# Performance work log

Hardware: AMD Instinct MI355X
Metric: run time of the kernel (lower is better)

Reference implementation:

```python
import jax, jax.numpy as jnp
import numpy as np

NUM_HEADS = 8
NEG_INF = -1e30


def _within_bucket_rank(idx):
    # idx: [U] int32 bucket ids; returns occurrence count of each id among earlier positions
    U = idx.shape[0]
    order = jnp.argsort(idx, stable=True)
    sv = idx[order]
    pos = jnp.arange(U, dtype=jnp.int32)
    is_start = jnp.concatenate([jnp.ones((1,), bool), sv[1:] != sv[:-1]])
    start = jax.lax.cummax(jnp.where(is_start, pos, 0))
    rank = pos - start
    return jnp.zeros(U, jnp.int32).at[order].set(rank)


def setup_inputs() -> dict:
    key = jax.random.key(0)
    ks = jax.random.split(key, 10)
    B, U, G, E = 8, 16384, 64, 128
    lin = jnp.linspace(0.0, 1.0, G)
    gx, gy = jnp.meshgrid(lin, lin, indexing='ij')
    xc_on_grid = jnp.broadcast_to(jnp.stack([gx, gy], -1), (B, G, G, 2)).astype(jnp.float32)
    s = 0.02
    return {
        'xc_off_grid': jax.random.uniform(ks[0], (B, U, 2), jnp.float32),
        'xc_on_grid': xc_on_grid,
        'zc_off_grid': jax.random.normal(ks[1], (B, U, E), jnp.float32),
        'zc_on_grid': jax.random.normal(ks[2], (B, G, G, E), jnp.float32),
        'latents': jax.random.normal(ks[3], (G * G, E), jnp.float32),
        'fake_embedding': jax.random.normal(ks[4], (E,), jnp.float32),
        'Wq': jax.random.normal(ks[5], (E, E), jnp.float32) * s,
        'Wk': jax.random.normal(ks[6], (E, E), jnp.float32) * s,
        'Wv': jax.random.normal(ks[7], (E, E), jnp.float32) * s,
        'Wo': jax.random.normal(ks[8], (E, E), jnp.float32) * s,
        'ignore_on_grid': 0,
    }


def _bucketize(xc_off_grid, xc_on_grid):
    # returns nearest flat grid index per off-grid point, shape [B, U] int32
    B = xc_off_grid.shape[0]
    dims = xc_on_grid.shape[1:-1]
    S = int(np.prod(dims))
    grid_shape = jnp.asarray(dims, jnp.float32)
    x_on = xc_on_grid.reshape(B, S, -1)
    xmin = x_on.min(axis=(0, 1))
    xmax = x_on.max(axis=(0, 1))
    spacing = (xmax - xmin) / (grid_shape - 1.0)
    nm = jnp.floor((xc_off_grid - xmin + spacing / 2) / spacing)
    nm = jnp.clip(nm, 0.0, grid_shape - 1.0)
    # strides as in the original: flip(cumprod([1, *dims])[:-1])
    strides = np.flip(np.cumprod(np.concatenate([[1], np.asarray(dims)]))[:-1]).astype(np.float32)
    return (nm * jnp.asarray(strides)).sum(-1).astype(jnp.int32)


def _mhca(latents_q, kv, valid, Wq, Wk, Wv, Wo):
    # latents_q: [N,1,E], kv: [N,P,E], valid: [N,P] bool
    N, P, E = kv.shape
    H, Dh = NUM_HEADS, E // NUM_HEADS
    q = (latents_q @ Wq).reshape(N, 1, H, Dh)
    k = (kv @ Wk).reshape(N, P, H, Dh)
    v = (kv @ Wv).reshape(N, P, H, Dh)
    scores = jnp.einsum('nqhd,nkhd->nhqk', q, k) / jnp.sqrt(jnp.asarray(Dh, q.dtype))
    scores = jnp.where(valid[:, None, None, :], scores, NEG_INF)
    attn = jax.nn.softmax(scores, axis=-1)
    out = jnp.einsum('nhqk,nkhd->nqhd', attn, v).reshape(N, 1, E)
    return out @ Wo


def reference(xc_off_grid, xc_on_grid, zc_off_grid, zc_on_grid, latents, fake_embedding, Wq, Wk, Wv, Wo, ignore_on_grid):
    B, U, E = zc_off_grid.shape
    dims = xc_on_grid.shape[1:-1]
    S = int(np.prod(dims))
    z_on = zc_on_grid.reshape(B, S, E)

    nearest_idx = _bucketize(xc_off_grid, xc_on_grid)          # [B, U]
    cumcount = jax.vmap(_within_bucket_rank)(nearest_idx)       # [B, U]
    flat_seg = (nearest_idx + jnp.arange(B, dtype=jnp.int32)[:, None] * S).reshape(-1)
    counts = jax.ops.segment_sum(jnp.ones(B * U, jnp.int32), flat_seg, num_segments=B * S)
    max_patch = int(jax.device_get(counts.max())) + 1           # +1 slot for on-grid/fake token

    # ragged scatter of off-grid tokens into padded per-bucket buffer
    grid_stacked = jnp.zeros((B * S, max_patch, E), zc_off_grid.dtype)
    grid_stacked = grid_stacked.at[flat_seg, cumcount.reshape(-1)].set(zc_off_grid.reshape(B * U, E))
    if ignore_on_grid:
        last = jnp.broadcast_to(fake_embedding, (B * S, E))
    else:
        last = z_on.reshape(B * S, E)
    grid_stacked = grid_stacked.at[:, -1].set(last)

    slot = jnp.arange(max_patch)
    valid = (slot[None, :] < counts[:, None]) | (slot[None, :] == max_patch - 1)  # [B*S, P]

    lat = jnp.broadcast_to(latents[None], (B, S, E)).reshape(B * S, 1, E)
    zc = _mhca(lat, grid_stacked, valid, Wq, Wk, Wv, Wo)        # [B*S, 1, E]
    return zc.reshape(B, *dims, E)
```

## Files before the change

### kernel.cpp

```cpp
#include <hip/hip_runtime.h>
#include <hip/hip_bf16.h>
#include <math.h>

namespace {
constexpr int B_  = 8;
constexpr int U_  = 16384;
constexpr int S_  = 4096;
constexpr int E_  = 128;
constexpr int NTOK  = B_ * U_;
constexpr int NCELL = B_ * S_;
constexpr int FUSED_GRID = 1024;
constexpr int CAP = 32;
constexpr int SWZ2 = 2 * 16384;
}

typedef __attribute__((ext_vector_type(8))) short bf16x8;
typedef __attribute__((ext_vector_type(4))) float f32x4;

__device__ inline unsigned short bf16rne(float x) {
  unsigned u = __float_as_uint(x);
  u = u + 0x7fffu + ((u >> 16) & 1u);
  return (unsigned short)(u >> 16);
}

__device__ inline bf16x8 pack8(float4 a, float4 b) {
  union { __hip_bfloat162 h; unsigned int u; } q0, q1, q2, q3;
  q0.h = __float22bfloat162_rn(make_float2(a.x, a.y));
  q1.h = __float22bfloat162_rn(make_float2(a.z, a.w));
  q2.h = __float22bfloat162_rn(make_float2(b.x, b.y));
  q3.h = __float22bfloat162_rn(make_float2(b.z, b.w));
  union { unsigned int u[4]; bf16x8 v; } r;
  r.u[0] = q0.u; r.u[1] = q1.u; r.u[2] = q2.u; r.u[3] = q3.u;
  return r.v;
}

__global__ __launch_bounds__(1024, 4) void setup_kernel(
    const float* __restrict__ Wq, const float* __restrict__ Wk,
    const float* __restrict__ Wv, const float* __restrict__ Wo,
    const float* __restrict__ latents, const float* __restrict__ xc_off,
    unsigned short* __restrict__ Wsw, unsigned short* __restrict__ QKt,
    int* __restrict__ cnt, int* __restrict__ sorted) {
  const int tid = threadIdx.x;

  if (blockIdx.x < 128) {
    __shared__ __align__(16) unsigned short wq[16384];
    __shared__ float wkt[128 * 129];
    __shared__ float qbuf[32 * 128];
    const int s0 = blockIdx.x * 32;

    for (int i = tid; i < 16384; i += 1024) {
      const int k = i >> 7, n = i & 127;
      wq[(((k >> 3) * 128 + n) << 3) + (k & 7)] = bf16rne(Wq[i]);
      wkt[(i & 127) * 129 + (i >> 7)] = Wk[i];
    }
    __syncthreads();

    const int wave = tid >> 6, lane = tid & 63;
    const int c = lane & 15, g = lane >> 4;
    if (wave < 2) {
      const int t0w = s0 + wave * 16;
      f32x4 acc[8];
#pragma unroll
      for (int i = 0; i < 8; ++i) acc[i] = {0.f, 0.f, 0.f, 0.f};
      const float* arow = latents + (size_t)(t0w + c) * E_ + g * 8;
      const bf16x8* bq = (const bf16x8*)wq;
#pragma unroll
      for (int ks = 0; ks < 4; ++ks) {
        float4 a0 = *(const float4*)(arow + ks * 32);
        float4 a1 = *(const float4*)(arow + ks * 32 + 4);
        bf16x8 af = pack8(a0, a1);
        const int bo = (ks * 4 + g) * 128 + c;
#pragma unroll
        for (int nt = 0; nt < 8; ++nt)
          acc[nt] = __builtin_amdgcn_mfma_f32_16x16x32_bf16(af, bq[bo + nt * 16], acc[nt], 0, 0, 0);
      }
#pragma unroll
      for (int nt = 0; nt < 8; ++nt)
#pragma unroll
        for (int r = 0; r < 4; ++r)
          qbuf[(wave * 16 + g * 4 + r) * 128 + nt * 16 + c] = acc[nt][r] * 0.25f;
    }
    __syncthreads();

#pragma unroll
    for (int k = 0; k < 32; ++k) {
      const int o = k * 1024 + tid;
      const int e = o & 127, h = (o >> 7) & 7, sl = o >> 10;
      float acc = 0.f;
#pragma unroll
      for (int j = 0; j < 16; ++j)
        acc = fmaf(wkt[(h * 16 + j) * 129 + e], qbuf[sl * 128 + h * 16 + j], acc);
      QKt[(size_t)(s0 + sl) * 1024 + (e >> 3) * 64 + h * 8 + (e & 7)] = bf16rne(acc);
    }
  } else {
    const int base = (blockIdx.x - 128) * 1024 + tid;
    const int stride = 128 * 1024;
    for (int i = base; i < SWZ2 + NTOK; i += stride) {
      if (i < SWZ2) {
        const int w = i >> 14, e = i & 16383;
        const int k = e >> 7, n = e & 127;
        const float* src = (w == 0) ? Wv : Wo;
        Wsw[w * 16384 + (((k >> 3) * 128 + n) << 3) + (k & 7)] = bf16rne(src[e]);
      } else {
        const int tok = i - SWZ2;
        const int b = tok >> 14;
        const float sp = 1.0f / 63.0f;
        const float half = sp * 0.5f;
        const float x0 = xc_off[(size_t)tok * 2 + 0];
        const float x1 = xc_off[(size_t)tok * 2 + 1];
        float n0 = floorf((x0 - 0.0f + half) / sp);
        float n1 = floorf((x1 - 0.0f + half) / sp);
        n0 = fminf(fmaxf(n0, 0.0f), 63.0f);
        n1 = fminf(fmaxf(n1, 0.0f), 63.0f);
        const int seg = b * S_ + (int)(n0 * 64.0f + n1);
        const int rank = atomicAdd(&cnt[seg], 1);
        if (rank < CAP) sorted[seg * CAP + rank] = tok;
      }
    }
  }
}

__global__ __launch_bounds__(512, 4) void fused_cells(
    const float* __restrict__ zc_off, const float* __restrict__ zc_on,
    const float* __restrict__ fake, const int* __restrict__ ignore_flag,
    const unsigned short* __restrict__ Wv_sw,
    const unsigned short* __restrict__ QKt, const int* __restrict__ cnt,
    const int* __restrict__ sorted, float* __restrict__ out) {
  __shared__ __align__(16) unsigned short wv[16384];
  __shared__ float wbuf[8][16][9];
  const int tid = threadIdx.x;
  {
    const uint4* sv = (const uint4*)Wv_sw;
    uint4* dv = (uint4*)wv;
#pragma unroll
    for (int i = 0; i < 4; ++i) dv[i * 512 + tid] = sv[i * 512 + tid];
  }
  const int ign = *ignore_flag;
  __syncthreads();

  const int wave = tid >> 6, lane = tid & 63;
  const int c = lane & 15, g = lane >> 4;
  const bf16x8* bv = (const bf16x8*)wv;

  for (int grp = blockIdx.x; grp < NCELL / 8; grp += FUSED_GRID) {
    const int cell = grp * 8 + wave;
    const int s = cell & (S_ - 1);
    const int base = cell * CAP;
    const int n_off = min(cnt[cell], CAP);
    const bf16x8* bqk = (const bf16x8*)(QKt + (size_t)s * 1024);

    float num_acc[8], den_acc[8];
#pragma unroll
    for (int i = 0; i < 8; ++i) { num_acc[i] = 0.f; den_acc[i] = 0.f; }

    const int chunks = (n_off + 16) >> 4;

    for (int ch = 0; ch < chunks; ++ch) {
      const int idx = ch * 16 + c;
      const float* arow;
      if (idx < n_off)       arow = zc_off + (size_t)sorted[base + idx] * E_;
      else if (idx == n_off) arow = ign ? fake : (zc_on + (size_t)cell * E_);
      else                   arow = zc_on;
      arow += g * 8;

      bf16x8 af[4];
#pragma unroll
      for (int ks = 0; ks < 4; ++ks) {
        float4 a0 = *(const float4*)(arow + ks * 32);
        float4 a1 = *(const float4*)(arow + ks * 32 + 4);
        af[ks] = pack8(a0, a1);
      }

      f32x4 aS = {0.f, 0.f, 0.f, 0.f};
#pragma unroll
      for (int ks = 0; ks < 4; ++ks)
        aS = __builtin_amdgcn_mfma_f32_16x16x32_bf16(af[ks], bqk[(ks * 4 + g) * 8 + (c & 7)], aS, 0, 0, 0);

      if (c < 8) {
#pragma unroll
        for (int r = 0; r < 4; ++r) {
          const int t = g * 4 + r;
          wbuf[wave][t][c] = (ch * 16 + t <= n_off) ? __expf(aS[r]) : 0.f;
        }
      }

#pragma unroll 2
      for (int h = 0; h < 8; ++h) {
        float wr[4];
#pragma unroll
        for (int r = 0; r < 4; ++r) wr[r] = wbuf[wave][g * 4 + r][h];

        const int bo = g * 128 + c + h * 16;
        f32x4 aV = {0.f, 0.f, 0.f, 0.f};
#pragma unroll
        for (int ks = 0; ks < 4; ++ks)
          aV = __builtin_amdgcn_mfma_f32_16x16x32_bf16(af[ks], bv[bo + ks * 512], aV, 0, 0, 0);

        float sv = 0.f, sd = 0.f;
#pragma unroll
        for (int r = 0; r < 4; ++r) { sv = fmaf(wr[r], aV[r], sv); sd += wr[r]; }
        num_acc[h] += sv;
        den_acc[h] += sd;
      }
    }

#pragma unroll
    for (int i = 0; i < 8; ++i) {
      num_acc[i] += __shfl_xor(num_acc[i], 16, 64);
      num_acc[i] += __shfl_xor(num_acc[i], 32, 64);
      den_acc[i] += __shfl_xor(den_acc[i], 16, 64);
      den_acc[i] += __shfl_xor(den_acc[i], 32, 64);
    }
#pragma unroll
    for (int b = 0; b < 2; ++b) {
      const int nt = 2 * g + b;
      out[(size_t)cell * E_ + nt * 16 + c] = num_acc[nt] / den_acc[nt];
    }
  }
}

__global__ __launch_bounds__(512, 4) void finalize_mfma(
    const unsigned short* __restrict__ Wo_sw, float* __restrict__ out) {
  __shared__ __align__(16) unsigned short wo[16384];
  const int tid = threadIdx.x;
  {
    const uint4* s = (const uint4*)Wo_sw;
    uint4* d = (uint4*)wo;
#pragma unroll
    for (int i = 0; i < 4; ++i) d[i * 512 + tid] = s[i * 512 + tid];
  }
  __syncthreads();

  const int wave = tid >> 6, lane = tid & 63;
  const int c = lane & 15, g = lane >> 4;
  const int t0w = blockIdx.x * 128 + wave * 16;

  f32x4 acc[8];
#pragma unroll
  for (int i = 0; i < 8; ++i) acc[i] = {0.f, 0.f, 0.f, 0.f};

  const float* nrow = out + (size_t)(t0w + c) * E_ + g * 8;
  const bf16x8* bo_ = (const bf16x8*)wo;
#pragma unroll
  for (int ks = 0; ks < 4; ++ks) {
    float4 a0 = *(const float4*)(nrow + ks * 32);
    float4 a1 = *(const float4*)(nrow + ks * 32 + 4);
    bf16x8 af = pack8(a0, a1);
    const int bofs = (ks * 4 + g) * 128 + c;
#pragma unroll
    for (int nt = 0; nt < 8; ++nt)
      acc[nt] = __builtin_amdgcn_mfma_f32_16x16x32_bf16(af, bo_[bofs + nt * 16], acc[nt], 0, 0, 0);
  }
#pragma unroll
  for (int nt = 0; nt < 8; ++nt)
#pragma unroll
    for (int r = 0; r < 4; ++r)
      out[(size_t)(t0w + g * 4 + r) * E_ + nt * 16 + c] = acc[nt][r];
}

extern "C" void kernel_launch(void* const* d_in, const int* in_sizes, int n_in,
                              void* d_out, int out_size, void* d_ws, size_t ws_size,
                              hipStream_t stream) {
  const float* xc_off  = (const float*)d_in[0];
  const float* zc_off  = (const float*)d_in[2];
  const float* zc_on   = (const float*)d_in[3];
  const float* latents = (const float*)d_in[4];
  const float* fake    = (const float*)d_in[5];
  const float* Wq      = (const float*)d_in[6];
  const float* Wk      = (const float*)d_in[7];
  const float* Wv      = (const float*)d_in[8];
  const float* Wo      = (const float*)d_in[9];
  const int*   ignore  = (const int*)d_in[10];

  float* out = (float*)d_out;

  unsigned short* QKt = (unsigned short*)d_ws;
  unsigned short* Wsw = QKt + (size_t)S_ * 1024;
  int* cnt    = (int*)(Wsw + SWZ2);
  int* sorted = cnt + NCELL;
  unsigned short* Wv_sw = Wsw;
  unsigned short* Wo_sw = Wsw + 16384;

  hipMemsetAsync(cnt, 0, NCELL * sizeof(int), stream);
  setup_kernel<<<256, 1024, 0, stream>>>(Wq, Wk, Wv, Wo, latents, xc_off,
                                         Wsw, QKt, cnt, sorted);
  fused_cells<<<FUSED_GRID, 512, 0, stream>>>(zc_off, zc_on, fake, ignore,
                                              Wv_sw, QKt, cnt, sorted, out);
  finalize_mfma<<<NCELL / 128, 512, 0, stream>>>(Wo_sw, out);
}
```

Measured before the change: 186.5 us.

## Rework setup QK projection split and pass attention weights via shuffles

The setup kernel's Q·Wk^T stage now uses 256 blocks of 16 latents each instead of 128 blocks of 32. It drops the transposed Wk shared-memory copy and instead has each thread load its Wk row slice into registers and compute vectorised dot products. The binning work gets 64 blocks instead of 128. In the fused attention kernel, the per-head exp weights move from a shared-memory buffer to registers and are broadcast with wavefront shuffles, removing LDS traffic and the shared buffer at the cost of shuffle instructions.

```diff
diff --git a/kernel.cpp b/kernel.cpp
--- a/kernel.cpp
+++ b/kernel.cpp
@@ -42,27 +42,24 @@
     int* __restrict__ cnt, int* __restrict__ sorted) {
   const int tid = threadIdx.x;
 
-  if (blockIdx.x < 128) {
+  if (blockIdx.x < 256) {
     __shared__ __align__(16) unsigned short wq[16384];
-    __shared__ float wkt[128 * 129];
-    __shared__ float qbuf[32 * 128];
-    const int s0 = blockIdx.x * 32;
+    __shared__ __align__(16) float qbuf[16 * 128];
+    const int s0 = blockIdx.x * 16;
 
     for (int i = tid; i < 16384; i += 1024) {
       const int k = i >> 7, n = i & 127;
       wq[(((k >> 3) * 128 + n) << 3) + (k & 7)] = bf16rne(Wq[i]);
-      wkt[(i & 127) * 129 + (i >> 7)] = Wk[i];
     }
     __syncthreads();
 
     const int wave = tid >> 6, lane = tid & 63;
-    const int c = lane & 15, g = lane >> 4;
-    if (wave < 2) {
-      const int t0w = s0 + wave * 16;
+    if (wave == 0) {
+      const int c = lane & 15, g = lane >> 4;
       f32x4 acc[8];
 #pragma unroll
       for (int i = 0; i < 8; ++i) acc[i] = {0.f, 0.f, 0.f, 0.f};
-      const float* arow = latents + (size_t)(t0w + c) * E_ + g * 8;
+      const float* arow = latents + (size_t)(s0 + c) * E_ + g * 8;
       const bf16x8* bq = (const bf16x8*)wq;
 #pragma unroll
       for (int ks = 0; ks < 4; ++ks) {
@@ -78,23 +75,32 @@
       for (int nt = 0; nt < 8; ++nt)
 #pragma unroll
         for (int r = 0; r < 4; ++r)
-          qbuf[(wave * 16 + g * 4 + r) * 128 + nt * 16 + c] = acc[nt][r] * 0.25f;
+          qbuf[(g * 4 + r) * 128 + nt * 16 + c] = acc[nt][r] * 0.25f;
     }
     __syncthreads();
 
-#pragma unroll
-    for (int k = 0; k < 32; ++k) {
-      const int o = k * 1024 + tid;
-      const int e = o & 127, h = (o >> 7) & 7, sl = o >> 10;
-      float acc = 0.f;
-#pragma unroll
-      for (int j = 0; j < 16; ++j)
-        acc = fmaf(wkt[(h * 16 + j) * 129 + e], qbuf[sl * 128 + h * 16 + j], acc);
-      QKt[(size_t)(s0 + sl) * 1024 + (e >> 3) * 64 + h * 8 + (e & 7)] = bf16rne(acc);
+    const int e = tid & 127, h = tid >> 7;
+    float4 w0 = *(const float4*)(Wk + (size_t)e * E_ + h * 16);
+    float4 w1 = *(const float4*)(Wk + (size_t)e * E_ + h * 16 + 4);
+    float4 w2 = *(const float4*)(Wk + (size_t)e * E_ + h * 16 + 8);
+    float4 w3 = *(const float4*)(Wk + (size_t)e * E_ + h * 16 + 12);
+    unsigned short* dst = QKt + (e >> 3) * 64 + h * 8 + (e & 7);
+#pragma unroll
+    for (int sl = 0; sl < 16; ++sl) {
+      const float* qp = qbuf + sl * 128 + h * 16;
+      float4 q0 = *(const float4*)(qp);
+      float4 q1 = *(const float4*)(qp + 4);
+      float4 q2 = *(const float4*)(qp + 8);
+      float4 q3 = *(const float4*)(qp + 12);
+      float acc = w0.x*q0.x + w0.y*q0.y + w0.z*q0.z + w0.w*q0.w
+                + w1.x*q1.x + w1.y*q1.y + w1.z*q1.z + w1.w*q1.w
+                + w2.x*q2.x + w2.y*q2.y + w2.z*q2.z + w2.w*q2.w
+                + w3.x*q3.x + w3.y*q3.y + w3.z*q3.z + w3.w*q3.w;
+      dst[(size_t)(s0 + sl) * 1024] = bf16rne(acc);
     }
   } else {
-    const int base = (blockIdx.x - 128) * 1024 + tid;
-    const int stride = 128 * 1024;
+    const int base = (blockIdx.x - 256) * 1024 + tid;
+    const int stride = 64 * 1024;
     for (int i = base; i < SWZ2 + NTOK; i += stride) {
       if (i < SWZ2) {
         const int w = i >> 14, e = i & 16383;
@@ -127,7 +133,6 @@
     const unsigned short* __restrict__ QKt, const int* __restrict__ cnt,
     const int* __restrict__ sorted, float* __restrict__ out) {
   __shared__ __align__(16) unsigned short wv[16384];
-  __shared__ float wbuf[8][16][9];
   const int tid = threadIdx.x;
   {
     const uint4* sv = (const uint4*)Wv_sw;
@@ -176,19 +181,18 @@
       for (int ks = 0; ks < 4; ++ks)
         aS = __builtin_amdgcn_mfma_f32_16x16x32_bf16(af[ks], bqk[(ks * 4 + g) * 8 + (c & 7)], aS, 0, 0, 0);
 
-      if (c < 8) {
-#pragma unroll
-        for (int r = 0; r < 4; ++r) {
-          const int t = g * 4 + r;
-          wbuf[wave][t][c] = (ch * 16 + t <= n_off) ? __expf(aS[r]) : 0.f;
-        }
+      float w_reg[4];
+#pragma unroll
+      for (int r = 0; r < 4; ++r) {
+        const int t = g * 4 + r;
+        w_reg[r] = (ch * 16 + t <= n_off) ? __expf(aS[r]) : 0.f;
       }
 
 #pragma unroll 2
       for (int h = 0; h < 8; ++h) {
         float wr[4];
 #pragma unroll
-        for (int r = 0; r < 4; ++r) wr[r] = wbuf[wave][g * 4 + r][h];
+        for (int r = 0; r < 4; ++r) wr[r] = __shfl(w_reg[r], (lane & 48) + h, 64);
 
         const int bo = g * 128 + c + h * 16;
         f32x4 aV = {0.f, 0.f, 0.f, 0.f};
@@ -282,7 +286,7 @@
   unsigned short* Wo_sw = Wsw + 16384;
 
   hipMemsetAsync(cnt, 0, NCELL * sizeof(int), stream);
-  setup_kernel<<<256, 1024, 0, stream>>>(Wq, Wk, Wv, Wo, latents, xc_off,
+  setup_kernel<<<320, 1024, 0, stream>>>(Wq, Wk, Wv, Wo, latents, xc_off,
                                          Wsw, QKt, cnt, sorted);
   fused_cells<<<FUSED_GRID, 512, 0, stream>>>(zc_off, zc_on, fake, ignore,
                                               Wv_sw, QKt, cnt, sorted, out);
```

New measurement: 187.0 us. Within noise of the previous version (+0.3%).
